# Kernel tuning notes

Hardware: AMD Instinct MI355X
Metric: run time of the kernel (lower is better)

The kernel has to match this reference:

```python
import jax, jax.numpy as jnp
import numpy as np
import math

D_MODEL = 512
NHEAD = 8
D_K = D_MODEL // NHEAD
WINDOW = 128
BATCH = 1
SEQ = 4096
NEG = -1e9  # matches torch masked_fill value


def setup_inputs() -> dict:
    key = jax.random.key(0)
    ks = jax.random.split(key, 9)
    s = 1.0 / math.sqrt(D_MODEL)
    return {
        "x": jax.random.normal(ks[0], (BATCH, SEQ, D_MODEL), dtype=jnp.float32),
        "wq": jax.random.uniform(ks[1], (D_MODEL, D_MODEL), jnp.float32, -s, s),
        "bq": jax.random.uniform(ks[2], (D_MODEL,), jnp.float32, -s, s),
        "wk": jax.random.uniform(ks[3], (D_MODEL, D_MODEL), jnp.float32, -s, s),
        "bk": jax.random.uniform(ks[4], (D_MODEL,), jnp.float32, -s, s),
        "wv": jax.random.uniform(ks[5], (D_MODEL, D_MODEL), jnp.float32, -s, s),
        "bv": jax.random.uniform(ks[6], (D_MODEL,), jnp.float32, -s, s),
        "wo": jax.random.uniform(ks[7], (D_MODEL, D_MODEL), jnp.float32, -s, s),
        "bo": jax.random.uniform(ks[8], (D_MODEL,), jnp.float32, -s, s),
    }


def reference(x, wq, bq, wk, bk, wv, bv, wo, bo):
    B, S, D = x.shape
    # projections -> (B, H, S, d_k)
    q = (x @ wq.T + bq).reshape(B, S, NHEAD, D_K).transpose(0, 2, 1, 3)
    k = (x @ wk.T + bk).reshape(B, S, NHEAD, D_K).transpose(0, 2, 1, 3)
    v = (x @ wv.T + bv).reshape(B, S, NHEAD, D_K).transpose(0, 2, 1, 3)
    # dense scores, band-masked (faithful to original: full S x S)
    scores = jnp.einsum('bhqd,bhkd->bhqk', q, k) / math.sqrt(D_K)
    idx = jnp.arange(S)
    band = jnp.abs(idx[:, None] - idx[None, :]) <= WINDOW  # (S, S)
    scores = jnp.where(band[None, None], scores, NEG)
    attn = jax.nn.softmax(scores, axis=-1)  # (B, H, S, S)
    ctx = jnp.einsum('bhqk,bhkd->bhqd', attn, v)
    ctx = ctx.transpose(0, 2, 1, 3).reshape(B, S, D)
    out = ctx @ wo.T + bo
    return out, attn
```

## Files before the change

kernel.cpp:

```cpp
#include <hip/hip_runtime.h>
#include <hip/hip_bf16.h>
#include <math.h>

#define S 4096
#define D 512
#define H 8
#define DK 64
#define WIN 128

typedef __attribute__((ext_vector_type(8))) short bf16x8;
typedef __attribute__((ext_vector_type(4))) float f32x4;

__device__ __forceinline__ unsigned short f2bf(float f) {
    __hip_bfloat16 h = __float2bfloat16(f);
    return *(unsigned short*)&h;
}

__global__ __launch_bounds__(256) void conv_bf16_kernel(
    const float* __restrict__ in, unsigned short* __restrict__ out, int n)
{
    const int i = (blockIdx.x * 256 + threadIdx.x) * 8;
    if (i >= n) return;
    float4 a = *(const float4*)&in[i];
    float4 b = *(const float4*)&in[i + 4];
    ushort4 o0 = {f2bf(a.x), f2bf(a.y), f2bf(a.z), f2bf(a.w)};
    ushort4 o1 = {f2bf(b.x), f2bf(b.y), f2bf(b.z), f2bf(b.w)};
    *(ushort4*)&out[i]     = o0;
    *(ushort4*)&out[i + 4] = o1;
}

__device__ __forceinline__ void mfma_gemm_body(
    const unsigned short* __restrict__ A,
    const float* __restrict__ W,
    const float* __restrict__ bias,
    float* __restrict__ C,
    unsigned short* __restrict__ CB)
{
    __shared__ unsigned short Bs[64][520];

    const int tid  = threadIdx.x;
    const int m0   = blockIdx.x * 128;
    const int n0   = blockIdx.y * 64;
    const int wv   = tid >> 6;
    const int lane = tid & 63;
    const int l16  = lane & 15;
    const int klo  = (lane >> 4) * 8;

    #pragma unroll
    for (int it = 0; it < 16; ++it) {
        const int c   = tid + it * 256;
        const int row = c >> 6;
        const int kc  = (c & 63) * 8;
        const float* src = &W[(size_t)(n0 + row) * 512 + kc];
        float4 a = *(const float4*)&src[0];
        float4 b = *(const float4*)&src[4];
        ushort4 o0 = {f2bf(a.x), f2bf(a.y), f2bf(a.z), f2bf(a.w)};
        ushort4 o1 = {f2bf(b.x), f2bf(b.y), f2bf(b.z), f2bf(b.w)};
        *(ushort4*)&Bs[row][kc]     = o0;
        *(ushort4*)&Bs[row][kc + 4] = o1;
    }
    __syncthreads();

    const unsigned short* arow0 = &A[(size_t)(m0 + wv * 32 + l16) * 512 + klo];
    const unsigned short* arow1 = arow0 + 16 * 512;

    f32x4 acc[2][4];
    #pragma unroll
    for (int r = 0; r < 2; ++r)
        #pragma unroll
        for (int nf = 0; nf < 4; ++nf)
            acc[r][nf] = (f32x4){0.f, 0.f, 0.f, 0.f};

    #pragma unroll 4
    for (int kb = 0; kb < 512; kb += 32) {
        bf16x8 a0 = *(const bf16x8*)&arow0[kb];
        bf16x8 a1 = *(const bf16x8*)&arow1[kb];
        #pragma unroll
        for (int nf = 0; nf < 4; ++nf) {
            bf16x8 b = *(const bf16x8*)&Bs[nf * 16 + l16][kb + klo];
            acc[0][nf] = __builtin_amdgcn_mfma_f32_16x16x32_bf16(a0, b, acc[0][nf], 0, 0, 0);
            acc[1][nf] = __builtin_amdgcn_mfma_f32_16x16x32_bf16(a1, b, acc[1][nf], 0, 0, 0);
        }
    }

    const int r0 = (lane >> 4) * 4;
    #pragma unroll
    for (int r = 0; r < 2; ++r) {
        #pragma unroll
        for (int nf = 0; nf < 4; ++nf) {
            const int col = n0 + nf * 16 + l16;
            const float bb = bias[col];
            #pragma unroll
            for (int vv = 0; vv < 4; ++vv) {
                const int row = m0 + wv * 32 + r * 16 + r0 + vv;
                const float val = acc[r][nf][vv] + bb;
                if (C)  C [(size_t)row * 512 + col] = val;
                if (CB) CB[(size_t)row * 512 + col] = f2bf(val);
            }
        }
    }
}

__global__ __launch_bounds__(256) void proj3_kernel(
    const unsigned short* __restrict__ xb,
    const float* __restrict__ wq, const float* __restrict__ bq,
    const float* __restrict__ wk, const float* __restrict__ bk,
    const float* __restrict__ wv, const float* __restrict__ bv,
    float* __restrict__ q, float* __restrict__ k, float* __restrict__ v)
{
    const float* W; const float* b; float* C;
    if (blockIdx.z == 0)      { W = wq; b = bq; C = q; }
    else if (blockIdx.z == 1) { W = wk; b = bk; C = k; }
    else                      { W = wv; b = bv; C = v; }
    mfma_gemm_body(xb, W, b, C, nullptr);
}

__global__ __launch_bounds__(256) void outproj_kernel(
    const unsigned short* __restrict__ ctxb,
    const float* __restrict__ wo, const float* __restrict__ bo,
    float* __restrict__ out)
{
    mfma_gemm_body(ctxb, wo, bo, out, nullptr);
}

__global__ __launch_bounds__(256) void band_attn_kernel(
    const float* __restrict__ q, const float* __restrict__ k,
    float* __restrict__ attn)
{
    __shared__ float Qs[64][20];
    __shared__ float Ks[64][68];
    __shared__ float P[16][336];
    __shared__ float rinvs[16];

    const int tid = threadIdx.x;
    const int h  = blockIdx.y;
    const int q0 = blockIdx.x * 16;
    const int w0 = q0 - 128;

    {
        const int row = tid & 15;
        const int db  = (tid >> 4) * 4;
        float4 a = *(const float4*)&q[(size_t)(q0 + row) * 512 + h * 64 + db];
        Qs[db + 0][row] = a.x; Qs[db + 1][row] = a.y;
        Qs[db + 2][row] = a.z; Qs[db + 3][row] = a.w;
    }

    const int lr = tid >> 2;
    const int ld = (tid & 3) * 16;
    const int rr = tid & 15;
    const int cc = (tid >> 4) * 4;

    for (int ch = 0; ch < 5; ++ch) {
        const int c0 = w0 + ch * 64;
        if (c0 + 64 <= 0 || c0 >= S) continue;
        __syncthreads();
        {
            const int krow = min(max(c0 + lr, 0), S - 1);
            #pragma unroll
            for (int t = 0; t < 4; ++t) {
                float4 v4 = *(const float4*)&k[(size_t)krow * 512 + h * 64 + ld + t * 4];
                Ks[ld + t * 4 + 0][lr] = v4.x;
                Ks[ld + t * 4 + 1][lr] = v4.y;
                Ks[ld + t * 4 + 2][lr] = v4.z;
                Ks[ld + t * 4 + 3][lr] = v4.w;
            }
        }
        __syncthreads();

        float sc[4] = {};
        #pragma unroll 8
        for (int d = 0; d < 64; ++d) {
            const float qa = Qs[d][rr];
            float4 kv = *(const float4*)&Ks[d][cc];
            sc[0] = fmaf(qa, kv.x, sc[0]);
            sc[1] = fmaf(qa, kv.y, sc[1]);
            sc[2] = fmaf(qa, kv.z, sc[2]);
            sc[3] = fmaf(qa, kv.w, sc[3]);
        }

        float4 o = {sc[0] * 0.125f, sc[1] * 0.125f,
                    sc[2] * 0.125f, sc[3] * 0.125f};
        *(float4*)&P[rr][ch * 64 + cc] = o;
    }
    __syncthreads();

    {
        const int r   = tid >> 4;
        const int l16 = tid & 15;
        const int i   = q0 + r;
        const int lo = max(i - WIN, 0) - w0;
        const int hi = min(i + WIN, S - 1) - w0;

        float m = -1e30f;
        for (int c = lo + l16; c <= hi; c += 16) m = fmaxf(m, P[r][c]);
        m = fmaxf(m, __shfl_xor(m, 1));
        m = fmaxf(m, __shfl_xor(m, 2));
        m = fmaxf(m, __shfl_xor(m, 4));
        m = fmaxf(m, __shfl_xor(m, 8));

        float sum = 0.f;
        for (int c = lo + l16; c <= hi; c += 16) {
            float e = __expf(P[r][c] - m);
            P[r][c] = e;
            sum += e;
        }
        sum += __shfl_xor(sum, 1);
        sum += __shfl_xor(sum, 2);
        sum += __shfl_xor(sum, 4);
        sum += __shfl_xor(sum, 8);
        if (l16 == 0) rinvs[r] = 1.0f / sum;
    }
    __syncthreads();

    float* rowbase = attn + (size_t)h * S * S;
    #pragma unroll 1
    for (int r = 0; r < 16; ++r) {
        const int i = q0 + r;
        float* rowp = rowbase + (size_t)i * S;
        const int lo = max(i - WIN, 0) - w0;
        const int hi = min(i + WIN, S - 1) - w0;
        const float rv = rinvs[r];
        #pragma unroll
        for (int t = 0; t < 4; ++t) {
            const int c4 = (tid + t * 256) << 2;
            const int lc = c4 - w0;
            float4 o;
            if (lc >= lo && lc + 3 <= hi) {
                float4 p = *(const float4*)&P[r][lc];
                o.x = p.x * rv; o.y = p.y * rv; o.z = p.z * rv; o.w = p.w * rv;
            } else if (lc + 3 < lo || lc > hi) {
                o = make_float4(0.f, 0.f, 0.f, 0.f);
            } else {
                o.x = (lc + 0 >= lo && lc + 0 <= hi) ? P[r][lc + 0] * rv : 0.f;
                o.y = (lc + 1 >= lo && lc + 1 <= hi) ? P[r][lc + 1] * rv : 0.f;
                o.z = (lc + 2 >= lo && lc + 2 <= hi) ? P[r][lc + 2] * rv : 0.f;
                o.w = (lc + 3 >= lo && lc + 3 <= hi) ? P[r][lc + 3] * rv : 0.f;
            }
            *(float4*)&rowp[c4] = o;
        }
    }
}

__global__ __launch_bounds__(256) void band_pv_kernel(
    const float* __restrict__ attn, const float* __restrict__ v,
    unsigned short* __restrict__ ctxb)
{
    __shared__ unsigned short Pb [64][328];
    __shared__ unsigned short VsT[64][328];
    const int tid = threadIdx.x;
    const int h  = blockIdx.y;
    const int q0 = blockIdx.x * 64;
    const int w0 = q0 - 128;

    const int lr = tid >> 2;
    const int ld = (tid & 3) * 16;
    const float* aptr = attn + (size_t)h * S * S;

    for (int ch = 0; ch < 5; ++ch) {
        const int c0 = w0 + ch * 64;
        if (c0 >= 0 && c0 < S) {
            #pragma unroll
            for (int t = 0; t < 4; ++t) {
                float4 p4 = *(const float4*)&aptr[(size_t)(q0 + lr) * S + c0 + ld + t * 4];
                ushort4 o = {f2bf(p4.x), f2bf(p4.y), f2bf(p4.z), f2bf(p4.w)};
                *(ushort4*)&Pb[lr][ch * 64 + ld + t * 4] = o;
                float4 v4 = *(const float4*)&v[(size_t)(c0 + lr) * 512 + h * 64 + ld + t * 4];
                VsT[ld + t * 4 + 0][ch * 64 + lr] = f2bf(v4.x);
                VsT[ld + t * 4 + 1][ch * 64 + lr] = f2bf(v4.y);
                VsT[ld + t * 4 + 2][ch * 64 + lr] = f2bf(v4.z);
                VsT[ld + t * 4 + 3][ch * 64 + lr] = f2bf(v4.w);
            }
        } else {
            #pragma unroll
            for (int t = 0; t < 4; ++t) {
                ushort4 z4 = {0, 0, 0, 0};
                *(ushort4*)&Pb[lr][ch * 64 + ld + t * 4] = z4;
                VsT[ld + t * 4 + 0][ch * 64 + lr] = 0;
                VsT[ld + t * 4 + 1][ch * 64 + lr] = 0;
                VsT[ld + t * 4 + 2][ch * 64 + lr] = 0;
                VsT[ld + t * 4 + 3][ch * 64 + lr] = 0;
            }
        }
    }
    __syncthreads();

    const int wv   = tid >> 6;
    const int lane = tid & 63;
    const int l16  = lane & 15;
    const int klo  = (lane >> 4) * 8;

    f32x4 acc[4];
    #pragma unroll
    for (int nf = 0; nf < 4; ++nf) acc[nf] = (f32x4){0.f, 0.f, 0.f, 0.f};

    #pragma unroll
    for (int ks = 0; ks < 10; ++ks) {
        bf16x8 a = *(const bf16x8*)&Pb[wv * 16 + l16][ks * 32 + klo];
        #pragma unroll
        for (int nf = 0; nf < 4; ++nf) {
            bf16x8 b = *(const bf16x8*)&VsT[nf * 16 + l16][ks * 32 + klo];
            acc[nf] = __builtin_amdgcn_mfma_f32_16x16x32_bf16(a, b, acc[nf], 0, 0, 0);
        }
    }

    const int r0 = (lane >> 4) * 4;
    #pragma unroll
    for (int nf = 0; nf < 4; ++nf) {
        #pragma unroll
        for (int vv = 0; vv < 4; ++vv) {
            const int row = q0 + wv * 16 + r0 + vv;
            ctxb[(size_t)row * 512 + h * 64 + nf * 16 + l16] = f2bf(acc[nf][vv]);
        }
    }
}

extern "C" void kernel_launch(void* const* d_in, const int* in_sizes, int n_in,
                              void* d_out, int out_size, void* d_ws, size_t ws_size,
                              hipStream_t stream)
{
    (void)in_sizes; (void)n_in; (void)out_size; (void)ws_size;
    const float* x  = (const float*)d_in[0];
    const float* wq = (const float*)d_in[1];
    const float* bq = (const float*)d_in[2];
    const float* wk = (const float*)d_in[3];
    const float* bk = (const float*)d_in[4];
    const float* wv = (const float*)d_in[5];
    const float* bv = (const float*)d_in[6];
    const float* wo = (const float*)d_in[7];
    const float* bo = (const float*)d_in[8];

    float* out  = (float*)d_out;
    float* attn = out + (size_t)S * D;

    float* q = (float*)d_ws;
    float* k = q + (size_t)S * D;
    float* v = k + (size_t)S * D;
    unsigned short* xb   = (unsigned short*)(v + (size_t)S * D);
    unsigned short* ctxb = xb + (size_t)S * D;

    conv_bf16_kernel<<<(S * D) / (256 * 8), 256, 0, stream>>>(x, xb, S * D);
    proj3_kernel<<<dim3(32, 8, 3), 256, 0, stream>>>(xb, wq, bq, wk, bk, wv, bv, q, k, v);
    band_attn_kernel<<<dim3(256, 8), 256, 0, stream>>>(q, k, attn);
    band_pv_kernel<<<dim3(64, 8), 256, 0, stream>>>(attn, v, ctxb);
    outproj_kernel<<<dim3(32, 8), 256, 0, stream>>>(ctxb, wo, bo, out);
}
```

Measured before the change: 173.2 us.

## Store Q/K/V as bf16 and compute band QK^T scores with MFMA

```diff
diff --git a/kernel.cpp b/kernel.cpp
--- a/kernel.cpp
+++ b/kernel.cpp
@@ -106,13 +106,14 @@
     const float* __restrict__ wq, const float* __restrict__ bq,
     const float* __restrict__ wk, const float* __restrict__ bk,
     const float* __restrict__ wv, const float* __restrict__ bv,
-    float* __restrict__ q, float* __restrict__ k, float* __restrict__ v)
-{
-    const float* W; const float* b; float* C;
-    if (blockIdx.z == 0)      { W = wq; b = bq; C = q; }
-    else if (blockIdx.z == 1) { W = wk; b = bk; C = k; }
-    else                      { W = wv; b = bv; C = v; }
-    mfma_gemm_body(xb, W, b, C, nullptr);
+    unsigned short* __restrict__ qb, unsigned short* __restrict__ kb,
+    unsigned short* __restrict__ vb)
+{
+    const float* W; const float* b; unsigned short* CB;
+    if (blockIdx.z == 0)      { W = wq; b = bq; CB = qb; }
+    else if (blockIdx.z == 1) { W = wk; b = bk; CB = kb; }
+    else                      { W = wv; b = bv; CB = vb; }
+    mfma_gemm_body(xb, W, b, nullptr, CB);
 }
 
 __global__ __launch_bounds__(256) void outproj_kernel(
@@ -124,11 +125,11 @@
 }
 
 __global__ __launch_bounds__(256) void band_attn_kernel(
-    const float* __restrict__ q, const float* __restrict__ k,
+    const unsigned short* __restrict__ qb, const unsigned short* __restrict__ kb,
     float* __restrict__ attn)
 {
-    __shared__ float Qs[64][20];
-    __shared__ float Ks[64][68];
+    __shared__ __align__(16) unsigned short Qs[16][72];
+    __shared__ __align__(16) unsigned short Kb[64][72];
     __shared__ float P[16][336];
     __shared__ float rinvs[16];
 
@@ -137,18 +138,21 @@
     const int q0 = blockIdx.x * 16;
     const int w0 = q0 - 128;
 
+    const int wv   = tid >> 6;
+    const int lane = tid & 63;
+    const int l16  = lane & 15;
+    const int klo  = (lane >> 4) * 8;
+    const int r0   = (lane >> 4) * 4;
+
     {
-        const int row = tid & 15;
-        const int db  = (tid >> 4) * 4;
-        float4 a = *(const float4*)&q[(size_t)(q0 + row) * 512 + h * 64 + db];
-        Qs[db + 0][row] = a.x; Qs[db + 1][row] = a.y;
-        Qs[db + 2][row] = a.z; Qs[db + 3][row] = a.w;
+        const int row = tid >> 4;
+        const int db  = (tid & 15) * 4;
+        *(ushort4*)&Qs[row][db] =
+            *(const ushort4*)&qb[(size_t)(q0 + row) * 512 + h * 64 + db];
     }
 
     const int lr = tid >> 2;
     const int ld = (tid & 3) * 16;
-    const int rr = tid & 15;
-    const int cc = (tid >> 4) * 4;
 
     for (int ch = 0; ch < 5; ++ch) {
         const int c0 = w0 + ch * 64;
@@ -156,50 +160,41 @@
         __syncthreads();
         {
             const int krow = min(max(c0 + lr, 0), S - 1);
-            #pragma unroll
-            for (int t = 0; t < 4; ++t) {
-                float4 v4 = *(const float4*)&k[(size_t)krow * 512 + h * 64 + ld + t * 4];
-                Ks[ld + t * 4 + 0][lr] = v4.x;
-                Ks[ld + t * 4 + 1][lr] = v4.y;
-                Ks[ld + t * 4 + 2][lr] = v4.z;
-                Ks[ld + t * 4 + 3][lr] = v4.w;
-            }
+            const unsigned short* src = &kb[(size_t)krow * 512 + h * 64 + ld];
+            *(bf16x8*)&Kb[lr][ld]     = *(const bf16x8*)&src[0];
+            *(bf16x8*)&Kb[lr][ld + 8] = *(const bf16x8*)&src[8];
         }
         __syncthreads();
 
-        float sc[4] = {};
-        #pragma unroll 8
-        for (int d = 0; d < 64; ++d) {
-            const float qa = Qs[d][rr];
-            float4 kv = *(const float4*)&Ks[d][cc];
-            sc[0] = fmaf(qa, kv.x, sc[0]);
-            sc[1] = fmaf(qa, kv.y, sc[1]);
-            sc[2] = fmaf(qa, kv.z, sc[2]);
-            sc[3] = fmaf(qa, kv.w, sc[3]);
-        }
-
-        float4 o = {sc[0] * 0.125f, sc[1] * 0.125f,
-                    sc[2] * 0.125f, sc[3] * 0.125f};
-        *(float4*)&P[rr][ch * 64 + cc] = o;
+        f32x4 acc = (f32x4){0.f, 0.f, 0.f, 0.f};
+        #pragma unroll
+        for (int kk = 0; kk < 64; kk += 32) {
+            bf16x8 a = *(const bf16x8*)&Qs[l16][kk + klo];
+            bf16x8 b = *(const bf16x8*)&Kb[wv * 16 + l16][kk + klo];
+            acc = __builtin_amdgcn_mfma_f32_16x16x32_bf16(a, b, acc, 0, 0, 0);
+        }
+        #pragma unroll
+        for (int vv = 0; vv < 4; ++vv)
+            P[r0 + vv][ch * 64 + wv * 16 + l16] = acc[vv] * 0.125f;
     }
     __syncthreads();
 
     {
         const int r   = tid >> 4;
-        const int l16 = tid & 15;
+        const int lx  = tid & 15;
         const int i   = q0 + r;
         const int lo = max(i - WIN, 0) - w0;
         const int hi = min(i + WIN, S - 1) - w0;
 
         float m = -1e30f;
-        for (int c = lo + l16; c <= hi; c += 16) m = fmaxf(m, P[r][c]);
+        for (int c = lo + lx; c <= hi; c += 16) m = fmaxf(m, P[r][c]);
         m = fmaxf(m, __shfl_xor(m, 1));
         m = fmaxf(m, __shfl_xor(m, 2));
         m = fmaxf(m, __shfl_xor(m, 4));
         m = fmaxf(m, __shfl_xor(m, 8));
 
         float sum = 0.f;
-        for (int c = lo + l16; c <= hi; c += 16) {
+        for (int c = lo + lx; c <= hi; c += 16) {
             float e = __expf(P[r][c] - m);
             P[r][c] = e;
             sum += e;
@@ -208,7 +203,7 @@
         sum += __shfl_xor(sum, 2);
         sum += __shfl_xor(sum, 4);
         sum += __shfl_xor(sum, 8);
-        if (l16 == 0) rinvs[r] = 1.0f / sum;
+        if (lx == 0) rinvs[r] = 1.0f / sum;
     }
     __syncthreads();
 
@@ -242,7 +237,7 @@
 }
 
 __global__ __launch_bounds__(256) void band_pv_kernel(
-    const float* __restrict__ attn, const float* __restrict__ v,
+    const float* __restrict__ attn, const unsigned short* __restrict__ vb,
     unsigned short* __restrict__ ctxb)
 {
     __shared__ unsigned short Pb [64][328];
@@ -264,11 +259,11 @@
                 float4 p4 = *(const float4*)&aptr[(size_t)(q0 + lr) * S + c0 + ld + t * 4];
                 ushort4 o = {f2bf(p4.x), f2bf(p4.y), f2bf(p4.z), f2bf(p4.w)};
                 *(ushort4*)&Pb[lr][ch * 64 + ld + t * 4] = o;
-                float4 v4 = *(const float4*)&v[(size_t)(c0 + lr) * 512 + h * 64 + ld + t * 4];
-                VsT[ld + t * 4 + 0][ch * 64 + lr] = f2bf(v4.x);
-                VsT[ld + t * 4 + 1][ch * 64 + lr] = f2bf(v4.y);
-                VsT[ld + t * 4 + 2][ch * 64 + lr] = f2bf(v4.z);
-                VsT[ld + t * 4 + 3][ch * 64 + lr] = f2bf(v4.w);
+                ushort4 v4 = *(const ushort4*)&vb[(size_t)(c0 + lr) * 512 + h * 64 + ld + t * 4];
+                VsT[ld + t * 4 + 0][ch * 64 + lr] = v4.x;
+                VsT[ld + t * 4 + 1][ch * 64 + lr] = v4.y;
+                VsT[ld + t * 4 + 2][ch * 64 + lr] = v4.z;
+                VsT[ld + t * 4 + 3][ch * 64 + lr] = v4.w;
             }
         } else {
             #pragma unroll
@@ -332,15 +327,15 @@
     float* out  = (float*)d_out;
     float* attn = out + (size_t)S * D;
 
-    float* q = (float*)d_ws;
-    float* k = q + (size_t)S * D;
-    float* v = k + (size_t)S * D;
-    unsigned short* xb   = (unsigned short*)(v + (size_t)S * D);
-    unsigned short* ctxb = xb + (size_t)S * D;
+    unsigned short* xb   = (unsigned short*)d_ws;
+    unsigned short* qb   = xb   + (size_t)S * D;
+    unsigned short* kb   = qb   + (size_t)S * D;
+    unsigned short* vb   = kb   + (size_t)S * D;
+    unsigned short* ctxb = vb   + (size_t)S * D;
 
     conv_bf16_kernel<<<(S * D) / (256 * 8), 256, 0, stream>>>(x, xb, S * D);
-    proj3_kernel<<<dim3(32, 8, 3), 256, 0, stream>>>(xb, wq, bq, wk, bk, wv, bv, q, k, v);
-    band_attn_kernel<<<dim3(256, 8), 256, 0, stream>>>(q, k, attn);
-    band_pv_kernel<<<dim3(64, 8), 256, 0, stream>>>(attn, v, ctxb);
+    proj3_kernel<<<dim3(32, 8, 3), 256, 0, stream>>>(xb, wq, bq, wk, bk, wv, bv, qb, kb, vb);
+    band_attn_kernel<<<dim3(256, 8), 256, 0, stream>>>(qb, kb, attn);
+    band_pv_kernel<<<dim3(64, 8), 256, 0, stream>>>(attn, vb, ctxb);
     outproj_kernel<<<dim3(32, 8), 256, 0, stream>>>(ctxb, wo, bo, out);
 }
```

New measurement: 159.3 us. 1.09x faster.
